# Performance work log

Measured on AMD Instinct MI355X. Metric: run time of the kernel, lower is better.

The kernel has to match this reference:

```python
import jax, jax.numpy as jnp
import numpy as np

B, T, C, H = 8, 2048, 256, 4
D = C // H  # head_dim = 64
SCALE = D ** -0.5


def setup_inputs() -> dict:
    key = jax.random.key(0)
    ks = jax.random.split(key, 5)
    return {
        "x": jax.random.normal(ks[0], (B, T, C), dtype=jnp.float32),
        "Wqkv": jax.random.normal(ks[1], (C, 3 * C), dtype=jnp.float32) * (C ** -0.5),
        "bqkv": jax.random.normal(ks[2], (3 * C,), dtype=jnp.float32) * 0.02,
        "Wproj": jax.random.normal(ks[3], (C, C), dtype=jnp.float32) * (C ** -0.5),
        "bproj": jax.random.normal(ks[4], (C,), dtype=jnp.float32) * 0.02,
    }


def reference(x, Wqkv, bqkv, Wproj, bproj):
    b, t, c = x.shape
    # QKV projection -> (3, B, H, T, D) matching torch permute(2,0,3,1,4)
    qkv = (x @ Wqkv + bqkv).reshape(b, t, 3, H, D)
    qkv = jnp.transpose(qkv, (2, 0, 3, 1, 4))
    q, k, v = qkv[0], qkv[1], qkv[2]  # each (B, H, T, D)
    # Full T x T scores (faithful to the original non-fused implementation)
    attn = jnp.einsum("bhqd,bhkd->bhqk", q, k) * SCALE
    causal = jnp.triu(jnp.ones((t, t), dtype=bool), k=1)  # True above diagonal
    attn = jnp.where(causal, -jnp.inf, attn)
    attn = jax.nn.softmax(attn, axis=-1)
    # dropout is identity in eval mode
    out = jnp.einsum("bhqk,bhkd->bhqd", attn, v)  # (B, H, T, D)
    out = jnp.transpose(out, (0, 2, 1, 3)).reshape(b, t, c)
    return out @ Wproj + bproj
```

## Files before the change

kernel.cpp:

```cpp
#include <hip/hip_runtime.h>
#include <hip/hip_bf16.h>
#include <math.h>

#define BATCH 8
#define SEQ   2048
#define CH    256
#define NH    4
#define HD    64
#define NQB   (SEQ / 64)
#define QSCALE 0.18033688011112042f

typedef short  bfrag __attribute__((ext_vector_type(8)));
typedef float  ffrag __attribute__((ext_vector_type(4)));
typedef unsigned short ushort_t;

__device__ __forceinline__ unsigned short f2bf(float f) {
    union { float f; unsigned int u; } v; v.f = f;
    unsigned int r = v.u + 0x7FFF + ((v.u >> 16) & 1);
    return (unsigned short)(r >> 16);
}
__device__ __forceinline__ unsigned int pack2(float a, float b) {
    const __hip_bfloat162 p = __float22bfloat162_rn(make_float2(a, b));
    return *(const unsigned int*)&p;
}

#define WQN (CH * 3 * CH)
#define WPN (CH * CH)

__global__ __launch_bounds__(256) void prep_kernel(
    const float* __restrict__ Wqkv, const float* __restrict__ Wproj,
    ushort_t* __restrict__ WqkvT, ushort_t* __restrict__ WprojT) {
    const int fid = blockIdx.x * 256 + threadIdx.x;
    if (fid < WQN) {
        const int n = fid >> 8, k = fid & 255;
        WqkvT[n * CH + k] = f2bf(Wqkv[k * (3 * CH) + n]);
    } else if (fid < WQN + WPN) {
        const int i = fid - WQN;
        const int n = i >> 8, k = i & 255;
        WprojT[n * CH + k] = f2bf(Wproj[k * CH + n]);
    }
}

#define GLS 72

__global__ __launch_bounds__(256) void qkv_mfma_kernel(
    const float* __restrict__ x, const ushort_t* __restrict__ Wt,
    const float* __restrict__ bias,
    ushort_t* __restrict__ Qb, ushort_t* __restrict__ Kb,
    ushort_t* __restrict__ Vtb) {
    __shared__ ushort_t smem[2 * 128 * GLS];
    ushort_t* As = smem;
    ushort_t* Bs = smem + 128 * GLS;

    const int tid = threadIdx.x;
    const int wv  = tid >> 6;
    const int ln  = tid & 63;
    const int l15 = ln & 15;
    const int l4  = ln >> 4;
    const int wr  = wv >> 1;
    const int wc  = wv & 1;
    const int n0  = blockIdx.x * 128;
    const int m0  = blockIdx.y * 128;

    ffrag acc[4][4];
    #pragma unroll
    for (int i = 0; i < 4; i++)
        #pragma unroll
        for (int j = 0; j < 4; j++) acc[i][j] = (ffrag){0.f, 0.f, 0.f, 0.f};

    for (int k0 = 0; k0 < CH; k0 += 64) {
        #pragma unroll
        for (int r = 0; r < 4; r++) {
            const int fid = tid + r * 256;
            const int row = fid >> 3, c8 = (fid & 7) * 8;
            const float* xp = &x[(size_t)(m0 + row) * CH + k0 + c8];
            const float4 va = *(const float4*)xp;
            const float4 vb = *(const float4*)(xp + 4);
            uint4 pk;
            pk.x = pack2(va.x, va.y); pk.y = pack2(va.z, va.w);
            pk.z = pack2(vb.x, vb.y); pk.w = pack2(vb.z, vb.w);
            *(uint4*)&As[row * GLS + c8] = pk;
            *(uint4*)&Bs[row * GLS + c8] = *(const uint4*)&Wt[(n0 + row) * CH + k0 + c8];
        }
        __syncthreads();
        #pragma unroll
        for (int kk = 0; kk < 64; kk += 32) {
            bfrag a[4], b[4];
            #pragma unroll
            for (int i = 0; i < 4; i++)
                a[i] = *(const bfrag*)&As[(wr * 64 + i * 16 + l15) * GLS + kk + l4 * 8];
            #pragma unroll
            for (int j = 0; j < 4; j++)
                b[j] = *(const bfrag*)&Bs[(wc * 64 + j * 16 + l15) * GLS + kk + l4 * 8];
            #pragma unroll
            for (int i = 0; i < 4; i++)
                #pragma unroll
                for (int j = 0; j < 4; j++)
                    acc[i][j] = __builtin_amdgcn_mfma_f32_16x16x32_bf16(a[i], b[j], acc[i][j], 0, 0, 0);
        }
        __syncthreads();
    }

    const int mat = n0 >> 8;
    const int b   = m0 >> 11;
    const int t0  = m0 & (SEQ - 1);
    ushort_t (*T)[136] = (ushort_t(*)[136])smem;

    if (mat < 2) {
        const float sc = (mat == 0) ? QSCALE : 1.0f;
        #pragma unroll
        for (int j = 0; j < 4; j++) {
            const int n_local = wc * 64 + j * 16 + l15;
            const float bj = bias[n0 + n_local];
            #pragma unroll
            for (int i = 0; i < 4; i++) {
                const int m_base = wr * 64 + i * 16 + l4 * 4;
                #pragma unroll
                for (int r = 0; r < 4; r++)
                    T[m_base + r][n_local] = f2bf((acc[i][j][r] + bj) * sc);
            }
        }
        __syncthreads();
        ushort_t* dst = (mat == 0) ? Qb : Kb;
        #pragma unroll
        for (int rr = 0; rr < 8; rr++) {
            const int fid = tid + rr * 256;
            const int row = fid >> 4;
            const int c8  = (fid & 15) * 8;
            const int n_glob = n0 + c8;
            const int h = (n_glob >> 6) & 3;
            const int d = n_glob & 63;
            *(uint4*)&dst[((size_t)((b * NH + h) * SEQ) + t0 + row) * HD + d] =
                *(const uint4*)&T[row][c8];
        }
    } else {
        #pragma unroll
        for (int j = 0; j < 4; j++) {
            const int n_local = wc * 64 + j * 16 + l15;
            const float bj = bias[n0 + n_local];
            #pragma unroll
            for (int i = 0; i < 4; i++) {
                const int m_base = wr * 64 + i * 16 + l4 * 4;
                ushort4 pk;
                pk.x = f2bf(acc[i][j][0] + bj);
                pk.y = f2bf(acc[i][j][1] + bj);
                pk.z = f2bf(acc[i][j][2] + bj);
                pk.w = f2bf(acc[i][j][3] + bj);
                *(ushort4*)&T[n_local][m_base] = pk;
            }
        }
        __syncthreads();
        #pragma unroll
        for (int rr = 0; rr < 8; rr++) {
            const int fid = tid + rr * 256;
            const int row = fid >> 4;
            const int c8  = (fid & 15) * 8;
            const int n_glob = n0 + row;
            const int h = (n_glob >> 6) & 3;
            const int d = n_glob & 63;
            *(uint4*)&Vtb[(size_t)((b * NH + h) * HD + d) * SEQ + t0 + c8] =
                *(const uint4*)&T[row][c8];
        }
    }
}

__global__ __launch_bounds__(256, 4) void attn_mfma_kernel(
    const ushort_t* __restrict__ Qb, const ushort_t* __restrict__ Kb,
    const ushort_t* __restrict__ Vtb, ushort_t* __restrict__ out) {
    __shared__ ushort_t Ps[64 * 64];
    __shared__ ushort_t KV[4 * 64 * 64];

    const int tid = threadIdx.x;
    const int wv  = tid >> 6;
    const int ln  = tid & 63;
    const int l15 = ln & 15;
    const int l4  = ln >> 4;
    const int e   = l15 & 7;

    const int L  = blockIdx.x;
    const int g  = L & 255;
    const int s4 = L >> 8;
    const int v  = g >> 5;
    const int qb = (s4 == 0) ? (31 - v) : (s4 == 1) ? (16 + v) : (s4 == 2) ? (15 - v) : v;
    const int bh = g & 31;
    const int b  = bh >> 2;
    const int h  = bh & 3;

    const ushort_t* Qp = Qb + ((size_t)(bh * SEQ + qb * 64 + wv * 16 + l15)) * HD + l4 * 8;
    const bfrag bq0 = *(const bfrag*)Qp;
    const bfrag bq1 = *(const bfrag*)(Qp + 32);

    const ushort_t* Kbase = Kb  + (size_t)bh * SEQ * HD;
    const ushort_t* Vbase = Vtb + (size_t)bh * HD * SEQ;
    const int srow  = tid >> 3;
    const int sc    = tid & 7;
    const int goffA = srow * 64 + sc * 8;
    const int voffA = srow * SEQ + sc * 8;
    const int soffA = srow * 64 + ((sc ^ (srow & 7)) * 8);

    const int kf0 = l15 * 64 + ((l4 ^ e) * 8);
    const int pf0 = (wv * 16 + l15) * 64 + ((l4 ^ e) * 8);
    const int pp = e >> 1;
    const int pwb = (wv * 16 + l15) * 64 + (((l4 >> 1) ^ (e & 1)) * 8) + (l4 & 1) * 4;

    uint4 kK0, kK1, kV0, kV1;
    kK0 = *(const uint4*)&Kbase[goffA];
    kK1 = *(const uint4*)&Kbase[goffA + 32 * 64];
    kV0 = *(const uint4*)&Vbase[voffA];
    kV1 = *(const uint4*)&Vbase[voffA + 32 * SEQ];
    *(uint4*)&KV[soffA]          = kK0;
    *(uint4*)&KV[soffA + 2048]   = kK1;
    *(uint4*)&KV[8192 + soffA]        = kV0;
    *(uint4*)&KV[8192 + soffA + 2048] = kV1;
    if (qb >= 1) {
        kK0 = *(const uint4*)&Kbase[4096 + goffA];
        kK1 = *(const uint4*)&Kbase[4096 + goffA + 32 * 64];
        kV0 = *(const uint4*)&Vbase[64 + voffA];
        kV1 = *(const uint4*)&Vbase[64 + voffA + 32 * SEQ];
    }

    ffrag o[4];
    #pragma unroll
    for (int n = 0; n < 4; n++) o[n] = (ffrag){0.f, 0.f, 0.f, 0.f};
    float m_q = -INFINITY;
    float l_q = 0.f;
    const int qg_l = qb * 64 + wv * 16 + l15;

    for (int kt = 0; kt <= qb; kt++) {
        if (kt > 0) {
            const int kb = (kt & 1) * 4096;
            *(uint4*)&KV[kb + soffA]          = kK0;
            *(uint4*)&KV[kb + soffA + 2048]   = kK1;
            *(uint4*)&KV[8192 + kb + soffA]        = kV0;
            *(uint4*)&KV[8192 + kb + soffA + 2048] = kV1;
            if (kt < qb) {
                const ushort_t* Kp  = Kbase + (kt + 1) * 4096;
                const ushort_t* Vtp = Vbase + (kt + 1) * 64;
                kK0 = *(const uint4*)&Kp[goffA];
                kK1 = *(const uint4*)&Kp[goffA + 32 * 64];
                kV0 = *(const uint4*)&Vtp[voffA];
                kV1 = *(const uint4*)&Vtp[voffA + 32 * SEQ];
            }
        }
        __syncthreads();

        const ushort_t* Kbuf = KV + (kt & 1) * 4096;
        const ushort_t* Vbuf = KV + 8192 + (kt & 1) * 4096;

        ffrag s[4];
        #pragma unroll
        for (int n = 0; n < 4; n++) {
            const bfrag ak0 = *(const bfrag*)&Kbuf[n * 1024 + kf0];
            const bfrag ak1 = *(const bfrag*)&Kbuf[n * 1024 + (kf0 ^ 32)];
            ffrag z = (ffrag){0.f, 0.f, 0.f, 0.f};
            z = __builtin_amdgcn_mfma_f32_16x16x32_bf16(ak0, bq0, z, 0, 0, 0);
            z = __builtin_amdgcn_mfma_f32_16x16x32_bf16(ak1, bq1, z, 0, 0, 0);
            s[n] = z;
        }
        if (kt == qb) {
            #pragma unroll
            for (int n = 0; n < 4; n++)
                #pragma unroll
                for (int r = 0; r < 4; r++)
                    if (kt * 64 + n * 16 + l4 * 4 + r > qg_l) s[n][r] = -INFINITY;
        }

        float mx = s[0][0];
        #pragma unroll
        for (int n = 0; n < 4; n++)
            #pragma unroll
            for (int r = 0; r < 4; r++) mx = fmaxf(mx, s[n][r]);
        mx = fmaxf(mx, __shfl_xor(mx, 16));
        mx = fmaxf(mx, __shfl_xor(mx, 32));
        const float mn = fmaxf(m_q, mx);
        const float alpha = __builtin_amdgcn_exp2f(m_q - mn);
        m_q = mn;

        float rs = 0.f;
        #pragma unroll
        for (int n = 0; n < 4; n++)
            #pragma unroll
            for (int r = 0; r < 4; r++) {
                const float p = __builtin_amdgcn_exp2f(s[n][r] - mn);
                s[n][r] = p;
                rs += p;
            }
        rs += __shfl_xor(rs, 16);
        rs += __shfl_xor(rs, 32);
        l_q = l_q * alpha + rs;

        #pragma unroll
        for (int n = 0; n < 4; n++) {
            uint2 pk;
            pk.x = pack2(s[n][0], s[n][1]);
            pk.y = pack2(s[n][2], s[n][3]);
            *(uint2*)&Ps[pwb + ((n ^ pp) << 4)] = pk;
        }

        #pragma unroll
        for (int r = 0; r < 4; r++) {
            const float ar = __shfl(alpha, l4 * 20 + r);
            #pragma unroll
            for (int n = 0; n < 4; n++) o[n][r] *= ar;
        }

        const bfrag ap0 = *(const bfrag*)&Ps[pf0];
        const bfrag ap1 = *(const bfrag*)&Ps[pf0 ^ 32];
        #pragma unroll
        for (int n = 0; n < 4; n++) {
            const bfrag bv0 = *(const bfrag*)&Vbuf[n * 1024 + kf0];
            const bfrag bv1 = *(const bfrag*)&Vbuf[n * 1024 + (kf0 ^ 32)];
            o[n] = __builtin_amdgcn_mfma_f32_16x16x32_bf16(ap0, bv0, o[n], 0, 0, 0);
            o[n] = __builtin_amdgcn_mfma_f32_16x16x32_bf16(ap1, bv1, o[n], 0, 0, 0);
        }
    }

    const int tg = qb * 64 + wv * 16 + l4 * 4;
    ushort_t* op = out + (size_t)(b * SEQ) * CH + h * HD;
    #pragma unroll
    for (int r = 0; r < 4; r++) {
        const float lr = __shfl(l_q, l4 * 20 + r);
        const float li = 1.0f / lr;
        #pragma unroll
        for (int n = 0; n < 4; n++)
            op[(size_t)(tg + r) * CH + n * 16 + l15] = f2bf(o[n][r] * li);
    }
}

__global__ __launch_bounds__(256) void proj_mfma_kernel(
    const ushort_t* __restrict__ Ab, const ushort_t* __restrict__ Wt,
    const float* __restrict__ bias, float* __restrict__ O) {
    __shared__ ushort_t smem[(128 + 64) * GLS];
    ushort_t* As = smem;
    ushort_t* Bs = smem + 128 * GLS;

    const int tid = threadIdx.x;
    const int wv  = tid >> 6;
    const int ln  = tid & 63;
    const int l15 = ln & 15;
    const int l4  = ln >> 4;
    const int wr  = wv >> 1;
    const int wc  = wv & 1;
    const int n0  = blockIdx.x * 64;
    const int m0  = blockIdx.y * 128;

    ffrag acc[4][2];
    #pragma unroll
    for (int i = 0; i < 4; i++)
        #pragma unroll
        for (int j = 0; j < 2; j++) acc[i][j] = (ffrag){0.f, 0.f, 0.f, 0.f};

    for (int k0 = 0; k0 < CH; k0 += 64) {
        #pragma unroll
        for (int r = 0; r < 4; r++) {
            const int fid = tid + r * 256;
            const int row = fid >> 3, c8 = (fid & 7) * 8;
            *(uint4*)&As[row * GLS + c8] = *(const uint4*)&Ab[(size_t)(m0 + row) * CH + k0 + c8];
        }
        #pragma unroll
        for (int r = 0; r < 2; r++) {
            const int fid = tid + r * 256;
            const int row = fid >> 3, c8 = (fid & 7) * 8;
            *(uint4*)&Bs[row * GLS + c8] = *(const uint4*)&Wt[(n0 + row) * CH + k0 + c8];
        }
        __syncthreads();
        #pragma unroll
        for (int kk = 0; kk < 64; kk += 32) {
            bfrag a[4], b[2];
            #pragma unroll
            for (int i = 0; i < 4; i++)
                a[i] = *(const bfrag*)&As[(wr * 64 + i * 16 + l15) * GLS + kk + l4 * 8];
            #pragma unroll
            for (int j = 0; j < 2; j++)
                b[j] = *(const bfrag*)&Bs[(wc * 32 + j * 16 + l15) * GLS + kk + l4 * 8];
            #pragma unroll
            for (int i = 0; i < 4; i++)
                #pragma unroll
                for (int j = 0; j < 2; j++)
                    acc[i][j] = __builtin_amdgcn_mfma_f32_16x16x32_bf16(a[i], b[j], acc[i][j], 0, 0, 0);
        }
        __syncthreads();
    }

    #pragma unroll
    for (int j = 0; j < 2; j++) {
        const int n = n0 + wc * 32 + j * 16 + l15;
        const float bj = bias[n];
        #pragma unroll
        for (int i = 0; i < 4; i++) {
            const int m = m0 + wr * 64 + i * 16 + l4 * 4;
            #pragma unroll
            for (int r = 0; r < 4; r++)
                O[(size_t)(m + r) * CH + n] = acc[i][j][r] + bj;
        }
    }
}

extern "C" void kernel_launch(void* const* d_in, const int* in_sizes, int n_in,
                              void* d_out, int out_size, void* d_ws, size_t ws_size,
                              hipStream_t stream) {
    const float* x     = (const float*)d_in[0];
    const float* Wqkv  = (const float*)d_in[1];
    const float* bqkv  = (const float*)d_in[2];
    const float* Wproj = (const float*)d_in[3];
    const float* bproj = (const float*)d_in[4];
    float* out = (float*)d_out;

    const size_t BHTD = (size_t)BATCH * NH * SEQ * HD;
    ushort_t* WqkvT  = (ushort_t*)d_ws;
    ushort_t* WprojT = WqkvT + (size_t)3 * CH * CH;
    ushort_t* Qb     = WprojT + (size_t)CH * CH;
    ushort_t* Kb     = Qb + BHTD;
    ushort_t* Vtb    = Kb + BHTD;
    ushort_t* attn_b = Vtb + BHTD;

    const int M = BATCH * SEQ;

    {
        const int total = WQN + WPN;
        prep_kernel<<<(total + 255) / 256, 256, 0, stream>>>(Wqkv, Wproj, WqkvT, WprojT);
    }
    {
        dim3 grid((3 * CH) / 128, M / 128);
        qkv_mfma_kernel<<<grid, 256, 0, stream>>>(x, WqkvT, bqkv, Qb, Kb, Vtb);
    }
    {
        attn_mfma_kernel<<<dim3(NQB * BATCH * NH), 256, 0, stream>>>(Qb, Kb, Vtb, attn_b);
    }
    {
        dim3 grid(CH / 64, M / 128);
        proj_mfma_kernel<<<grid, 256, 0, stream>>>(attn_b, WprojT, bproj, out);
    }
}
```

Measured before the change: 144.2 us.

## Process two query tiles per attention block and prefetch GEMM operand tiles

The attention kernel now gives each block a 128-row query tile, split into two 64-row halves. Each K/V tile loaded into shared memory serves both halves, which halves K/V traffic and the number of blocks, at the cost of more registers and a lower occupancy bound. The QKV GEMM prefetches the next k-slice into registers before computing on the current one. The projection GEMM uses smaller 64x64 tiles with double-buffered shared memory and register prefetch, giving more blocks at the cost of less reuse per block.

```diff
diff --git a/kernel.cpp b/kernel.cpp
--- a/kernel.cpp
+++ b/kernel.cpp
@@ -7,7 +7,6 @@
 #define CH    256
 #define NH    4
 #define HD    64
-#define NQB   (SEQ / 64)
 #define QSCALE 0.18033688011112042f
 
 typedef short  bfrag __attribute__((ext_vector_type(8)));
@@ -68,21 +67,42 @@
         #pragma unroll
         for (int j = 0; j < 4; j++) acc[i][j] = (ffrag){0.f, 0.f, 0.f, 0.f};
 
-    for (int k0 = 0; k0 < CH; k0 += 64) {
+    float4 pa0[4], pa1[4];
+    uint4  pbv[4];
+    #pragma unroll
+    for (int r = 0; r < 4; r++) {
+        const int fid = tid + r * 256;
+        const int row = fid >> 3, c8 = (fid & 7) * 8;
+        const float* xp = &x[(size_t)(m0 + row) * CH + c8];
+        pa0[r] = *(const float4*)xp;
+        pa1[r] = *(const float4*)(xp + 4);
+        pbv[r] = *(const uint4*)&Wt[(n0 + row) * CH + c8];
+    }
+
+    for (int s = 0; s < 4; s++) {
         #pragma unroll
         for (int r = 0; r < 4; r++) {
             const int fid = tid + r * 256;
             const int row = fid >> 3, c8 = (fid & 7) * 8;
-            const float* xp = &x[(size_t)(m0 + row) * CH + k0 + c8];
-            const float4 va = *(const float4*)xp;
-            const float4 vb = *(const float4*)(xp + 4);
             uint4 pk;
-            pk.x = pack2(va.x, va.y); pk.y = pack2(va.z, va.w);
-            pk.z = pack2(vb.x, vb.y); pk.w = pack2(vb.z, vb.w);
+            pk.x = pack2(pa0[r].x, pa0[r].y); pk.y = pack2(pa0[r].z, pa0[r].w);
+            pk.z = pack2(pa1[r].x, pa1[r].y); pk.w = pack2(pa1[r].z, pa1[r].w);
             *(uint4*)&As[row * GLS + c8] = pk;
-            *(uint4*)&Bs[row * GLS + c8] = *(const uint4*)&Wt[(n0 + row) * CH + k0 + c8];
-        }
-        __syncthreads();
+            *(uint4*)&Bs[row * GLS + c8] = pbv[r];
+        }
+        __syncthreads();
+        if (s < 3) {
+            const int k0 = (s + 1) * 64;
+            #pragma unroll
+            for (int r = 0; r < 4; r++) {
+                const int fid = tid + r * 256;
+                const int row = fid >> 3, c8 = (fid & 7) * 8;
+                const float* xp = &x[(size_t)(m0 + row) * CH + k0 + c8];
+                pa0[r] = *(const float4*)xp;
+                pa1[r] = *(const float4*)(xp + 4);
+                pbv[r] = *(const uint4*)&Wt[(n0 + row) * CH + k0 + c8];
+            }
+        }
         #pragma unroll
         for (int kk = 0; kk < 64; kk += 32) {
             bfrag a[4], b[4];
@@ -164,10 +184,10 @@
     }
 }
 
-__global__ __launch_bounds__(256, 4) void attn_mfma_kernel(
+__global__ __launch_bounds__(256, 2) void attn_mfma_kernel(
     const ushort_t* __restrict__ Qb, const ushort_t* __restrict__ Kb,
     const ushort_t* __restrict__ Vtb, ushort_t* __restrict__ out) {
-    __shared__ ushort_t Ps[64 * 64];
+    __shared__ ushort_t Ps[128 * 64];
     __shared__ ushort_t KV[4 * 64 * 64];
 
     const int tid = threadIdx.x;
@@ -178,17 +198,18 @@
     const int e   = l15 & 7;
 
     const int L  = blockIdx.x;
-    const int g  = L & 255;
-    const int s4 = L >> 8;
-    const int v  = g >> 5;
-    const int qb = (s4 == 0) ? (31 - v) : (s4 == 1) ? (16 + v) : (s4 == 2) ? (15 - v) : v;
-    const int bh = g & 31;
+    const int u  = L >> 5;
+    const int bh = L & 31;
+    const int qt = (u < 8) ? (15 - u) : (u - 8);
     const int b  = bh >> 2;
     const int h  = bh & 3;
-
-    const ushort_t* Qp = Qb + ((size_t)(bh * SEQ + qb * 64 + wv * 16 + l15)) * HD + l4 * 8;
-    const bfrag bq0 = *(const bfrag*)Qp;
-    const bfrag bq1 = *(const bfrag*)(Qp + 32);
+    const int ktmax = 2 * qt + 1;
+
+    const ushort_t* Qp0 = Qb + ((size_t)(bh * SEQ + qt * 128 + wv * 16 + l15)) * HD + l4 * 8;
+    const bfrag bq00 = *(const bfrag*)Qp0;
+    const bfrag bq01 = *(const bfrag*)(Qp0 + 32);
+    const bfrag bq10 = *(const bfrag*)(Qp0 + 64 * HD);
+    const bfrag bq11 = *(const bfrag*)(Qp0 + 64 * HD + 32);
 
     const ushort_t* Kbase = Kb  + (size_t)bh * SEQ * HD;
     const ushort_t* Vbase = Vtb + (size_t)bh * HD * SEQ;
@@ -200,44 +221,44 @@
 
     const int kf0 = l15 * 64 + ((l4 ^ e) * 8);
     const int pf0 = (wv * 16 + l15) * 64 + ((l4 ^ e) * 8);
-    const int pp = e >> 1;
+    const int pp  = e >> 1;
     const int pwb = (wv * 16 + l15) * 64 + (((l4 >> 1) ^ (e & 1)) * 8) + (l4 & 1) * 4;
 
-    uint4 kK0, kK1, kV0, kV1;
-    kK0 = *(const uint4*)&Kbase[goffA];
-    kK1 = *(const uint4*)&Kbase[goffA + 32 * 64];
-    kV0 = *(const uint4*)&Vbase[voffA];
-    kV1 = *(const uint4*)&Vbase[voffA + 32 * SEQ];
-    *(uint4*)&KV[soffA]          = kK0;
-    *(uint4*)&KV[soffA + 2048]   = kK1;
+    uint4 kK0 = *(const uint4*)&Kbase[goffA];
+    uint4 kK1 = *(const uint4*)&Kbase[goffA + 2048];
+    uint4 kV0 = *(const uint4*)&Vbase[voffA];
+    uint4 kV1 = *(const uint4*)&Vbase[voffA + 32 * SEQ];
+    *(uint4*)&KV[soffA]               = kK0;
+    *(uint4*)&KV[soffA + 2048]        = kK1;
     *(uint4*)&KV[8192 + soffA]        = kV0;
     *(uint4*)&KV[8192 + soffA + 2048] = kV1;
-    if (qb >= 1) {
-        kK0 = *(const uint4*)&Kbase[4096 + goffA];
-        kK1 = *(const uint4*)&Kbase[4096 + goffA + 32 * 64];
-        kV0 = *(const uint4*)&Vbase[64 + voffA];
-        kV1 = *(const uint4*)&Vbase[64 + voffA + 32 * SEQ];
-    }
-
-    ffrag o[4];
-    #pragma unroll
-    for (int n = 0; n < 4; n++) o[n] = (ffrag){0.f, 0.f, 0.f, 0.f};
-    float m_q = -INFINITY;
-    float l_q = 0.f;
-    const int qg_l = qb * 64 + wv * 16 + l15;
-
-    for (int kt = 0; kt <= qb; kt++) {
+    kK0 = *(const uint4*)&Kbase[4096 + goffA];
+    kK1 = *(const uint4*)&Kbase[4096 + goffA + 2048];
+    kV0 = *(const uint4*)&Vbase[64 + voffA];
+    kV1 = *(const uint4*)&Vbase[64 + voffA + 32 * SEQ];
+
+    ffrag o0[4], o1[4];
+    #pragma unroll
+    for (int n = 0; n < 4; n++) {
+        o0[n] = (ffrag){0.f, 0.f, 0.f, 0.f};
+        o1[n] = (ffrag){0.f, 0.f, 0.f, 0.f};
+    }
+    float m0q = -INFINITY, l0q = 0.f;
+    float m1q = -INFINITY, l1q = 0.f;
+    const int rel = wv * 16 + l15;
+
+    for (int kt = 0; kt <= ktmax; kt++) {
         if (kt > 0) {
             const int kb = (kt & 1) * 4096;
-            *(uint4*)&KV[kb + soffA]          = kK0;
-            *(uint4*)&KV[kb + soffA + 2048]   = kK1;
+            *(uint4*)&KV[kb + soffA]               = kK0;
+            *(uint4*)&KV[kb + soffA + 2048]        = kK1;
             *(uint4*)&KV[8192 + kb + soffA]        = kV0;
             *(uint4*)&KV[8192 + kb + soffA + 2048] = kV1;
-            if (kt < qb) {
+            if (kt < ktmax) {
                 const ushort_t* Kp  = Kbase + (kt + 1) * 4096;
                 const ushort_t* Vtp = Vbase + (kt + 1) * 64;
                 kK0 = *(const uint4*)&Kp[goffA];
-                kK1 = *(const uint4*)&Kp[goffA + 32 * 64];
+                kK1 = *(const uint4*)&Kp[goffA + 2048];
                 kV0 = *(const uint4*)&Vtp[voffA];
                 kV1 = *(const uint4*)&Vtp[voffA + 32 * SEQ];
             }
@@ -247,92 +268,167 @@
         const ushort_t* Kbuf = KV + (kt & 1) * 4096;
         const ushort_t* Vbuf = KV + 8192 + (kt & 1) * 4096;
 
-        ffrag s[4];
+        bfrag ak0[4], ak1[4];
         #pragma unroll
         for (int n = 0; n < 4; n++) {
-            const bfrag ak0 = *(const bfrag*)&Kbuf[n * 1024 + kf0];
-            const bfrag ak1 = *(const bfrag*)&Kbuf[n * 1024 + (kf0 ^ 32)];
-            ffrag z = (ffrag){0.f, 0.f, 0.f, 0.f};
-            z = __builtin_amdgcn_mfma_f32_16x16x32_bf16(ak0, bq0, z, 0, 0, 0);
-            z = __builtin_amdgcn_mfma_f32_16x16x32_bf16(ak1, bq1, z, 0, 0, 0);
-            s[n] = z;
-        }
-        if (kt == qb) {
+            ak0[n] = *(const bfrag*)&Kbuf[n * 1024 + kf0];
+            ak1[n] = *(const bfrag*)&Kbuf[n * 1024 + (kf0 ^ 32)];
+        }
+
+        const bool act0 = (kt <= 2 * qt);
+        const bool dia0 = (kt == 2 * qt);
+        const bool dia1 = (kt == ktmax);
+
+        if (act0) {
+            ffrag s[4];
+            #pragma unroll
+            for (int n = 0; n < 4; n++) {
+                ffrag z = (ffrag){0.f, 0.f, 0.f, 0.f};
+                z = __builtin_amdgcn_mfma_f32_16x16x32_bf16(ak0[n], bq00, z, 0, 0, 0);
+                z = __builtin_amdgcn_mfma_f32_16x16x32_bf16(ak1[n], bq01, z, 0, 0, 0);
+                s[n] = z;
+            }
+            if (dia0) {
+                #pragma unroll
+                for (int n = 0; n < 4; n++)
+                    #pragma unroll
+                    for (int r = 0; r < 4; r++)
+                        if (n * 16 + l4 * 4 + r > rel) s[n][r] = -INFINITY;
+            }
+            float mx = s[0][0];
             #pragma unroll
             for (int n = 0; n < 4; n++)
                 #pragma unroll
-                for (int r = 0; r < 4; r++)
-                    if (kt * 64 + n * 16 + l4 * 4 + r > qg_l) s[n][r] = -INFINITY;
-        }
-
-        float mx = s[0][0];
-        #pragma unroll
-        for (int n = 0; n < 4; n++)
-            #pragma unroll
-            for (int r = 0; r < 4; r++) mx = fmaxf(mx, s[n][r]);
-        mx = fmaxf(mx, __shfl_xor(mx, 16));
-        mx = fmaxf(mx, __shfl_xor(mx, 32));
-        const float mn = fmaxf(m_q, mx);
-        const float alpha = __builtin_amdgcn_exp2f(m_q - mn);
-        m_q = mn;
-
-        float rs = 0.f;
-        #pragma unroll
-        for (int n = 0; n < 4; n++)
+                for (int r = 0; r < 4; r++) mx = fmaxf(mx, s[n][r]);
+            mx = fmaxf(mx, __shfl_xor(mx, 16));
+            mx = fmaxf(mx, __shfl_xor(mx, 32));
+            const float mn = fmaxf(m0q, mx);
+            const float alpha = __builtin_amdgcn_exp2f(m0q - mn);
+            m0q = mn;
+            float rs = 0.f;
+            #pragma unroll
+            for (int n = 0; n < 4; n++)
+                #pragma unroll
+                for (int r = 0; r < 4; r++) {
+                    const float p = __builtin_amdgcn_exp2f(s[n][r] - mn);
+                    s[n][r] = p;
+                    rs += p;
+                }
+            rs += __shfl_xor(rs, 16);
+            rs += __shfl_xor(rs, 32);
+            l0q = l0q * alpha + rs;
+            #pragma unroll
+            for (int n = 0; n < 4; n++) {
+                uint2 pk;
+                pk.x = pack2(s[n][0], s[n][1]);
+                pk.y = pack2(s[n][2], s[n][3]);
+                *(uint2*)&Ps[pwb + ((n ^ pp) << 4)] = pk;
+            }
             #pragma unroll
             for (int r = 0; r < 4; r++) {
-                const float p = __builtin_amdgcn_exp2f(s[n][r] - mn);
-                s[n][r] = p;
-                rs += p;
-            }
-        rs += __shfl_xor(rs, 16);
-        rs += __shfl_xor(rs, 32);
-        l_q = l_q * alpha + rs;
-
-        #pragma unroll
-        for (int n = 0; n < 4; n++) {
-            uint2 pk;
-            pk.x = pack2(s[n][0], s[n][1]);
-            pk.y = pack2(s[n][2], s[n][3]);
-            *(uint2*)&Ps[pwb + ((n ^ pp) << 4)] = pk;
-        }
-
-        #pragma unroll
-        for (int r = 0; r < 4; r++) {
-            const float ar = __shfl(alpha, l4 * 20 + r);
-            #pragma unroll
-            for (int n = 0; n < 4; n++) o[n][r] *= ar;
-        }
-
-        const bfrag ap0 = *(const bfrag*)&Ps[pf0];
-        const bfrag ap1 = *(const bfrag*)&Ps[pf0 ^ 32];
+                const float ar = __shfl(alpha, l4 * 20 + r);
+                #pragma unroll
+                for (int n = 0; n < 4; n++) o0[n][r] *= ar;
+            }
+        }
+
+        {
+            ffrag s[4];
+            #pragma unroll
+            for (int n = 0; n < 4; n++) {
+                ffrag z = (ffrag){0.f, 0.f, 0.f, 0.f};
+                z = __builtin_amdgcn_mfma_f32_16x16x32_bf16(ak0[n], bq10, z, 0, 0, 0);
+                z = __builtin_amdgcn_mfma_f32_16x16x32_bf16(ak1[n], bq11, z, 0, 0, 0);
+                s[n] = z;
+            }
+            if (dia1) {
+                #pragma unroll
+                for (int n = 0; n < 4; n++)
+                    #pragma unroll
+                    for (int r = 0; r < 4; r++)
+                        if (n * 16 + l4 * 4 + r > rel) s[n][r] = -INFINITY;
+            }
+            float mx = s[0][0];
+            #pragma unroll
+            for (int n = 0; n < 4; n++)
+                #pragma unroll
+                for (int r = 0; r < 4; r++) mx = fmaxf(mx, s[n][r]);
+            mx = fmaxf(mx, __shfl_xor(mx, 16));
+            mx = fmaxf(mx, __shfl_xor(mx, 32));
+            const float mn = fmaxf(m1q, mx);
+            const float alpha = __builtin_amdgcn_exp2f(m1q - mn);
+            m1q = mn;
+            float rs = 0.f;
+            #pragma unroll
+            for (int n = 0; n < 4; n++)
+                #pragma unroll
+                for (int r = 0; r < 4; r++) {
+                    const float p = __builtin_amdgcn_exp2f(s[n][r] - mn);
+                    s[n][r] = p;
+                    rs += p;
+                }
+            rs += __shfl_xor(rs, 16);
+            rs += __shfl_xor(rs, 32);
+            l1q = l1q * alpha + rs;
+            #pragma unroll
+            for (int n = 0; n < 4; n++) {
+                uint2 pk;
+                pk.x = pack2(s[n][0], s[n][1]);
+                pk.y = pack2(s[n][2], s[n][3]);
+                *(uint2*)&Ps[4096 + pwb + ((n ^ pp) << 4)] = pk;
+            }
+            #pragma unroll
+            for (int r = 0; r < 4; r++) {
+                const float ar = __shfl(alpha, l4 * 20 + r);
+                #pragma unroll
+                for (int n = 0; n < 4; n++) o1[n][r] *= ar;
+            }
+        }
+
+        bfrag ap00, ap01;
+        if (act0) {
+            ap00 = *(const bfrag*)&Ps[pf0];
+            ap01 = *(const bfrag*)&Ps[pf0 ^ 32];
+        }
+        const bfrag ap10 = *(const bfrag*)&Ps[4096 + pf0];
+        const bfrag ap11 = *(const bfrag*)&Ps[4096 + (pf0 ^ 32)];
         #pragma unroll
         for (int n = 0; n < 4; n++) {
             const bfrag bv0 = *(const bfrag*)&Vbuf[n * 1024 + kf0];
             const bfrag bv1 = *(const bfrag*)&Vbuf[n * 1024 + (kf0 ^ 32)];
-            o[n] = __builtin_amdgcn_mfma_f32_16x16x32_bf16(ap0, bv0, o[n], 0, 0, 0);
-            o[n] = __builtin_amdgcn_mfma_f32_16x16x32_bf16(ap1, bv1, o[n], 0, 0, 0);
-        }
-    }
-
-    const int tg = qb * 64 + wv * 16 + l4 * 4;
+            if (act0) {
+                o0[n] = __builtin_amdgcn_mfma_f32_16x16x32_bf16(ap00, bv0, o0[n], 0, 0, 0);
+                o0[n] = __builtin_amdgcn_mfma_f32_16x16x32_bf16(ap01, bv1, o0[n], 0, 0, 0);
+            }
+            o1[n] = __builtin_amdgcn_mfma_f32_16x16x32_bf16(ap10, bv0, o1[n], 0, 0, 0);
+            o1[n] = __builtin_amdgcn_mfma_f32_16x16x32_bf16(ap11, bv1, o1[n], 0, 0, 0);
+        }
+    }
+
+    const int tg0 = qt * 128 + wv * 16 + l4 * 4;
     ushort_t* op = out + (size_t)(b * SEQ) * CH + h * HD;
     #pragma unroll
     for (int r = 0; r < 4; r++) {
-        const float lr = __shfl(l_q, l4 * 20 + r);
+        const float lr = __shfl(l0q, l4 * 20 + r);
         const float li = 1.0f / lr;
         #pragma unroll
         for (int n = 0; n < 4; n++)
-            op[(size_t)(tg + r) * CH + n * 16 + l15] = f2bf(o[n][r] * li);
+            op[(size_t)(tg0 + r) * CH + n * 16 + l15] = f2bf(o0[n][r] * li);
+    }
+    #pragma unroll
+    for (int r = 0; r < 4; r++) {
+        const float lr = __shfl(l1q, l4 * 20 + r);
+        const float li = 1.0f / lr;
+        #pragma unroll
+        for (int n = 0; n < 4; n++)
+            op[(size_t)(tg0 + 64 + r) * CH + n * 16 + l15] = f2bf(o1[n][r] * li);
     }
 }
 
 __global__ __launch_bounds__(256) void proj_mfma_kernel(
     const ushort_t* __restrict__ Ab, const ushort_t* __restrict__ Wt,
     const float* __restrict__ bias, float* __restrict__ O) {
-    __shared__ ushort_t smem[(128 + 64) * GLS];
-    ushort_t* As = smem;
-    ushort_t* Bs = smem + 128 * GLS;
+    __shared__ ushort_t smem[2 * 128 * GLS];
 
     const int tid = threadIdx.x;
     const int wv  = tid >> 6;
@@ -342,42 +438,52 @@
     const int wr  = wv >> 1;
     const int wc  = wv & 1;
     const int n0  = blockIdx.x * 64;
-    const int m0  = blockIdx.y * 128;
-
-    ffrag acc[4][2];
-    #pragma unroll
-    for (int i = 0; i < 4; i++)
+    const int m0  = blockIdx.y * 64;
+
+    const int srow = tid >> 3;
+    const int sc8  = (tid & 7) * 8;
+
+    ffrag acc[2][2];
+    #pragma unroll
+    for (int i = 0; i < 2; i++)
         #pragma unroll
         for (int j = 0; j < 2; j++) acc[i][j] = (ffrag){0.f, 0.f, 0.f, 0.f};
 
-    for (int k0 = 0; k0 < CH; k0 += 64) {
-        #pragma unroll
-        for (int r = 0; r < 4; r++) {
-            const int fid = tid + r * 256;
-            const int row = fid >> 3, c8 = (fid & 7) * 8;
-            *(uint4*)&As[row * GLS + c8] = *(const uint4*)&Ab[(size_t)(m0 + row) * CH + k0 + c8];
-        }
-        #pragma unroll
-        for (int r = 0; r < 2; r++) {
-            const int fid = tid + r * 256;
-            const int row = fid >> 3, c8 = (fid & 7) * 8;
-            *(uint4*)&Bs[row * GLS + c8] = *(const uint4*)&Wt[(n0 + row) * CH + k0 + c8];
-        }
-        __syncthreads();
+    uint4 ra0, ra1, rb0, rb1;
+    ra0 = *(const uint4*)&Ab[(size_t)(m0 + srow) * CH + sc8];
+    ra1 = *(const uint4*)&Ab[(size_t)(m0 + 32 + srow) * CH + sc8];
+    rb0 = *(const uint4*)&Wt[(n0 + srow) * CH + sc8];
+    rb1 = *(const uint4*)&Wt[(n0 + 32 + srow) * CH + sc8];
+
+    for (int s = 0; s < 4; s++) {
+        ushort_t* As = smem + (s & 1) * (128 * GLS);
+        ushort_t* Bs = As + 64 * GLS;
+        *(uint4*)&As[srow * GLS + sc8]        = ra0;
+        *(uint4*)&As[(32 + srow) * GLS + sc8] = ra1;
+        *(uint4*)&Bs[srow * GLS + sc8]        = rb0;
+        *(uint4*)&Bs[(32 + srow) * GLS + sc8] = rb1;
+        __syncthreads();
+        if (s < 3) {
+            const int k0 = (s + 1) * 64;
+            ra0 = *(const uint4*)&Ab[(size_t)(m0 + srow) * CH + k0 + sc8];
+            ra1 = *(const uint4*)&Ab[(size_t)(m0 + 32 + srow) * CH + k0 + sc8];
+            rb0 = *(const uint4*)&Wt[(n0 + srow) * CH + k0 + sc8];
+            rb1 = *(const uint4*)&Wt[(n0 + 32 + srow) * CH + k0 + sc8];
+        }
         #pragma unroll
         for (int kk = 0; kk < 64; kk += 32) {
-            bfrag a[4], b[2];
-            #pragma unroll
-            for (int i = 0; i < 4; i++)
-                a[i] = *(const bfrag*)&As[(wr * 64 + i * 16 + l15) * GLS + kk + l4 * 8];
+            bfrag a[2], bfr[2];
+            #pragma unroll
+            for (int i = 0; i < 2; i++)
+                a[i] = *(const bfrag*)&As[(wr * 32 + i * 16 + l15) * GLS + kk + l4 * 8];
             #pragma unroll
             for (int j = 0; j < 2; j++)
-                b[j] = *(const bfrag*)&Bs[(wc * 32 + j * 16 + l15) * GLS + kk + l4 * 8];
-            #pragma unroll
-            for (int i = 0; i < 4; i++)
+                bfr[j] = *(const bfrag*)&Bs[(wc * 32 + j * 16 + l15) * GLS + kk + l4 * 8];
+            #pragma unroll
+            for (int i = 0; i < 2; i++)
                 #pragma unroll
                 for (int j = 0; j < 2; j++)
-                    acc[i][j] = __builtin_amdgcn_mfma_f32_16x16x32_bf16(a[i], b[j], acc[i][j], 0, 0, 0);
+                    acc[i][j] = __builtin_amdgcn_mfma_f32_16x16x32_bf16(a[i], bfr[j], acc[i][j], 0, 0, 0);
         }
         __syncthreads();
     }
@@ -387,8 +493,8 @@
         const int n = n0 + wc * 32 + j * 16 + l15;
         const float bj = bias[n];
         #pragma unroll
-        for (int i = 0; i < 4; i++) {
-            const int m = m0 + wr * 64 + i * 16 + l4 * 4;
+        for (int i = 0; i < 2; i++) {
+            const int m = m0 + wr * 32 + i * 16 + l4 * 4;
             #pragma unroll
             for (int r = 0; r < 4; r++)
                 O[(size_t)(m + r) * CH + n] = acc[i][j][r] + bj;
@@ -425,10 +531,10 @@
         qkv_mfma_kernel<<<grid, 256, 0, stream>>>(x, WqkvT, bqkv, Qb, Kb, Vtb);
     }
     {
-        attn_mfma_kernel<<<dim3(NQB * BATCH * NH), 256, 0, stream>>>(Qb, Kb, Vtb, attn_b);
+        attn_mfma_kernel<<<dim3(512), 256, 0, stream>>>(Qb, Kb, Vtb, attn_b);
     }
     {
-        dim3 grid(CH / 64, M / 128);
+        dim3 grid(CH / 64, M / 64);
         proj_mfma_kernel<<<grid, 256, 0, stream>>>(attn_b, WprojT, bproj, out);
     }
 }
```

Result: slower. 249.5 us (+73.1%).
